# Kernel tuning notes

Measured on AMD Instinct MI355X. Metric: run time of the kernel, lower is better.

## Reference

```python
import jax, jax.numpy as jnp
import numpy as np

VOCAB = 32000
E = 512      # embed_dim
H = 512      # hidden_dim (== embed_dim, required by the output-averaging slice)
NUM_LAYERS = 2
WIN = 8
S = 512      # seq_len
B = 8        # batch


def setup_inputs() -> dict:
    key = jax.random.key(0)
    ks = jax.random.split(key, 40)
    d = {"encoder_input": jax.random.randint(ks[0], (S, B), 0, VOCAB, dtype=jnp.int64
                                             if jax.config.jax_enable_x64 else jnp.int32)}
    d["embed_table"] = jax.random.normal(ks[1], (VOCAB, E), jnp.float32) * 0.02
    i = 2
    for l in range(NUM_LAYERS):
        in_dim = E if l == 0 else 2 * H
        for dirn in ("f", "b"):
            sc = 1.0 / np.sqrt(H).astype(np.float32)
            d[f"wih{l}{dirn}"] = jax.random.normal(ks[i], (4 * H, in_dim), jnp.float32) * sc; i += 1
            d[f"whh{l}{dirn}"] = jax.random.normal(ks[i], (4 * H, H), jnp.float32) * sc; i += 1
            d[f"b{l}{dirn}"] = jax.random.normal(ks[i], (4 * H,), jnp.float32) * sc; i += 1
    return d


def _lstm_dir(x, mask, wih, whh, b, reverse):
    """One LSTM direction over padded windows. x: [L, N, in], mask: [L, N, 1].
    Masked (out-of-window) steps carry state unchanged; since invalid steps form a
    prefix in scan order (left pad for fwd, right pad for bwd-reversed), the zero
    initial state is preserved until the first valid step -> identical math to
    running the LSTM on the truncated window, as in the original per-token loop."""
    Hh = whh.shape[1]

    def step(carry, inp):
        h, c = carry
        xt, mt = inp
        g = xt @ wih.T + h @ whh.T + b                      # [N, 4H], torch gate order i,f,g,o
        i_, f_, g_, o_ = jnp.split(g, 4, axis=-1)
        c_new = jax.nn.sigmoid(f_) * c + jax.nn.sigmoid(i_) * jnp.tanh(g_)
        h_new = jax.nn.sigmoid(o_) * jnp.tanh(c_new)
        h = jnp.where(mt, h_new, h)
        c = jnp.where(mt, c_new, c)
        return (h, c), h

    N = x.shape[1]
    h0 = jnp.zeros((N, Hh), x.dtype)
    _, ys = jax.lax.scan(step, (h0, h0), (x, mask), reverse=reverse)
    return ys  # [L, N, Hh]


def _forward(encoder_input, embed_table, layer_params):
    S_, B_ = encoder_input.shape
    L = 2 * WIN + 1
    emb = embed_table[encoder_input]                         # [S, B, E]
    offs = jnp.arange(L) - WIN
    pos = jnp.arange(S_)[:, None] + offs[None, :]            # [S, L]
    valid = (pos >= 0) & (pos < S_)
    pidx = jnp.clip(pos, 0, S_ - 1)
    windows = emb[pidx]                                      # [S, L, B, E]
    x = windows.transpose(1, 0, 2, 3).reshape(L, S_ * B_, E)  # [L, N, E]
    mask = jnp.broadcast_to(valid.T[:, :, None, None], (L, S_, B_, 1)).reshape(L, S_ * B_, 1)
    for (wf, hf, bf, wb, hb, bb) in layer_params:
        yf = _lstm_dir(x, mask, wf, hf, bf, reverse=False)
        yb = _lstm_dir(x, mask, wb, hb, bb, reverse=True)
        x = jnp.concatenate([yf, yb], axis=-1)               # [L, N, 2H]
    out = x[WIN].reshape(S_, B_, 2 * H)                      # [S, B, 2H]
    return (out[:, :, :E] + out[:, :, E:]) / 2


def reference(encoder_input, embed_table,
              wih0f, whh0f, b0f, wih0b, whh0b, b0b,
              wih1f, whh1f, b1f, wih1b, whh1b, b1b):
    layer_params = [(wih0f, whh0f, b0f, wih0b, whh0b, b0b),
                    (wih1f, whh1f, b1f, wih1b, whh1b, b1b)]
    return _forward(encoder_input, embed_table, layer_params)
```

## Files before the change

kernel.cpp:

```cpp
#include <hip/hip_runtime.h>
#include <stdint.h>

typedef __bf16 bf16;
typedef __bf16 bf16x8 __attribute__((ext_vector_type(8)));
typedef __bf16 bf16x4 __attribute__((ext_vector_type(4)));
typedef float f32x4 __attribute__((ext_vector_type(4)));

#define WIN 8

__device__ __forceinline__ float sigm(float x) { return 1.0f / (1.0f + __expf(-x)); }
__device__ __forceinline__ float tanhfast(float x) { return 2.0f / (1.0f + __expf(-2.0f * x)) - 1.0f; }

__device__ __forceinline__ void gload16(const void* g, void* l) {
    __builtin_amdgcn_global_load_lds((const __attribute__((address_space(1))) void*)g,
                                     (__attribute__((address_space(3))) void*)l, 16, 0, 0);
}

struct StepArgs {
    const bf16* A1;
    const bf16* A2;
    const bf16* W;
    const float* bias;
    const bf16* P0;
    float* Cst;
    bf16* Hout;
    float* Hf32;
    const bf16* Hprev;
    int l;
    int firstStep;
};

template<int MODE>
__global__ __launch_bounds__(512, 2)
void step_pair(StepArgs fa, StepArgs ba) {
    const StepArgs a = blockIdx.z ? ba : fa;
    __shared__ alignas(16) char lds[131072];

    constexpr int SA1 = (MODE == 0) ? 512 : 1024;
    constexpr int SW  = (MODE == 2) ? 1536 : 512;
    constexpr int SH  = (MODE == 0) ? 2048 : (MODE == 1 ? 1024 : 512);
    constexpr int SHP = (MODE == 1) ? 1024 : 512;

    const int tid = threadIdx.x;
    const int w = tid >> 6;
    const int lane = tid & 63;
    const int wm = w >> 2, wn = w & 3;
    const int bx = blockIdx.x, by = blockIdx.y;
    const int rowBase = bx * 256;

    int KB;
    if (MODE == 0) KB = 8;
    else if (MODE == 1) KB = a.firstStep ? 0 : 8;
    else KB = a.firstStep ? 16 : 24;

    const int lq = lane >> 3;
    const int lc = lane & 7;
    const int swz = 8 * (lc ^ lq);

    const bf16* aP[4];
    const bf16* a2P[4];
    const bf16* bP[4];
#pragma unroll
    for (int q = 0; q < 4; ++q) {
        const int r = w * 32 + q * 8 + lq;
        const int n = rowBase + r;
        aP[q] = a.A1 ? (a.A1 + (size_t)n * SA1 + swz) : (const bf16*)0;
        if (MODE == 2) a2P[q] = a.A2 ? (a.A2 + (size_t)n * 512 + swz) : (const bf16*)0;
        int wr;
        if (MODE == 0) wr = by * 256 + r;
        else wr = ((r & 63) >> 4) * 512 + by * 64 + (r >> 6) * 16 + (r & 15);
        bP[q] = a.W + (size_t)wr * SW + swz;
    }

    const int l15 = lane & 15, l4 = lane >> 4;
    const int key = (l15 & 7) << 4;
    const int aBase = (wm * 128 + l15) * 128;
    const int bBase = (wn * 64 + l15) * 128;

    f32x4 acc[8][4];
    const f32x4 zf = {0.f, 0.f, 0.f, 0.f};
#pragma unroll
    for (int m = 0; m < 8; ++m)
#pragma unroll
        for (int n = 0; n < 4; ++n) acc[m][n] = zf;

    auto STAGE = [&](int buf, int kb) {
        char* Ad = lds + buf * 65536;
        char* Bd = Ad + 32768;
        const int ke = kb * 64;
        const int ldsOff0 = w * 32 * 128;
#pragma unroll
        for (int q = 0; q < 4; ++q) {
            const int ldsOff = ldsOff0 + q * 1024;
            const bf16* srcA;
            if (MODE == 2) srcA = (kb < 16) ? (aP[q] + ke) : (a2P[q] + (ke - 1024));
            else srcA = aP[q] + ke;
            gload16(srcA, Ad + ldsOff);
            gload16(bP[q] + ke, Bd + ldsOff);
        }
    };

    if (KB > 0) {
        STAGE(0, 0);
        for (int t = 0; t < KB; ++t) {
            const int cur = t & 1;
            if (t + 1 < KB) {
                STAGE(cur ^ 1, t + 1);
                asm volatile("s_waitcnt vmcnt(8)" ::: "memory");
            } else {
                asm volatile("s_waitcnt vmcnt(0)" ::: "memory");
            }
            __builtin_amdgcn_s_barrier();
            __builtin_amdgcn_sched_barrier(0);
            const char* Ab = lds + cur * 65536;
            const char* Bb = Ab + 32768;
            __builtin_amdgcn_s_setprio(1);
#pragma unroll
            for (int kk = 0; kk < 2; ++kk) {
                const int ko = (kk * 64 + l4 * 16) ^ key;
                bf16x8 af[8], bv[4];
#pragma unroll
                for (int m = 0; m < 8; ++m)
                    af[m] = *(const bf16x8*)(Ab + aBase + m * 2048 + ko);
#pragma unroll
                for (int n = 0; n < 4; ++n)
                    bv[n] = *(const bf16x8*)(Bb + bBase + n * 2048 + ko);
#pragma unroll
                for (int m = 0; m < 8; ++m)
#pragma unroll
                    for (int n = 0; n < 4; ++n)
                        acc[m][n] = __builtin_amdgcn_mfma_f32_16x16x32_bf16(af[m], bv[n], acc[m][n], 0, 0, 0);
            }
            __builtin_amdgcn_s_setprio(0);
            __builtin_amdgcn_sched_barrier(0);
            __builtin_amdgcn_s_barrier();
        }
    }

    if (MODE == 0) {
#pragma unroll
        for (int m = 0; m < 8; ++m)
#pragma unroll
            for (int n = 0; n < 4; ++n) {
                const int col = by * 256 + wn * 64 + n * 16 + l15;
#pragma unroll
                for (int e = 0; e < 4; ++e) {
                    const int row = rowBase + wm * 128 + m * 16 + l4 * 4 + e;
                    a.Hout[(size_t)row * SH + col] = (bf16)acc[m][n][e];
                }
            }
        return;
    }

    const int u = by * 64 + wn * 16 + l15;
    const float bi = a.bias[u];
    const float bff = a.bias[512 + u];
    const float bg = a.bias[1024 + u];
    const float bo = a.bias[1536 + u];
#pragma unroll
    for (int m = 0; m < 8; ++m) {
#pragma unroll
        for (int e = 0; e < 4; ++e) {
            const int n = rowBase + wm * 128 + m * 16 + l4 * 4 + e;
            const int s = n >> 3;
            const int p = s + a.l - WIN;
            const bool valid = ((unsigned)p < 512u);
            float gi = acc[m][0][e] + bi;
            float gf = acc[m][1][e] + bff;
            float gg = acc[m][2][e] + bg;
            float go = acc[m][3][e] + bo;
            if (MODE == 1) {
                const int pc = p < 0 ? 0 : (p > 511 ? 511 : p);
                const size_t pr = (size_t)(pc * 8 + (n & 7)) * 2048;
                gi += (float)a.P0[pr + u];
                gf += (float)a.P0[pr + 512 + u];
                gg += (float)a.P0[pr + 1024 + u];
                go += (float)a.P0[pr + 1536 + u];
            }
            const float cold = a.firstStep ? 0.0f : a.Cst[(size_t)n * 512 + u];
            const float cnew = sigm(gf) * cold + sigm(gi) * tanhfast(gg);
            const float hnew = sigm(go) * tanhfast(cnew);
            float hv, cv;
            if (valid) { hv = hnew; cv = cnew; }
            else {
                hv = a.Hprev ? (float)a.Hprev[(size_t)n * SHP + u] : 0.0f;
                cv = cold;
            }
            a.Cst[(size_t)n * 512 + u] = cv;
            a.Hout[(size_t)n * SH + u] = (bf16)hv;
            if (a.Hf32) a.Hf32[(size_t)n * 512 + u] = hv;
        }
    }
}

__global__ void embed_kernel(const int* __restrict__ tok, const float* __restrict__ tbl,
                             bf16* __restrict__ X0) {
    const int n = blockIdx.x;
    const int t = tok[n];
    const float4 v = ((const float4*)(tbl + (size_t)t * 512))[threadIdx.x];
    bf16x4 o = {(bf16)v.x, (bf16)v.y, (bf16)v.z, (bf16)v.w};
    ((bf16x4*)(X0 + (size_t)n * 512))[threadIdx.x] = o;
}

__global__ void cvt_kernel(const float* __restrict__ src, bf16* __restrict__ dst, int n4) {
    const int i = blockIdx.x * 256 + threadIdx.x;
    if (i < n4) {
        const float4 v = ((const float4*)src)[i];
        bf16x4 o = {(bf16)v.x, (bf16)v.y, (bf16)v.z, (bf16)v.w};
        ((bf16x4*)dst)[i] = o;
    }
}

__global__ void build_w1_kernel(const float* __restrict__ wih, const float* __restrict__ whh,
                                bf16* __restrict__ dst) {
    const int r = blockIdx.x;
    for (int k = threadIdx.x; k < 1536; k += 256) {
        const float v = (k < 1024) ? wih[(size_t)r * 1024 + k] : whh[(size_t)r * 512 + (k - 1024)];
        dst[(size_t)r * 1536 + k] = (bf16)v;
    }
}

__global__ void combine_kernel(const float* __restrict__ hf, const float* __restrict__ hb,
                               float* __restrict__ out) {
    const int i = blockIdx.x * 256 + threadIdx.x;
    const float4 x = ((const float4*)hf)[i];
    const float4 y = ((const float4*)hb)[i];
    float4 r;
    r.x = (x.x + y.x) * 0.5f;
    r.y = (x.y + y.y) * 0.5f;
    r.z = (x.z + y.z) * 0.5f;
    r.w = (x.w + y.w) * 0.5f;
    ((float4*)out)[i] = r;
}

extern "C" void kernel_launch(void* const* d_in, const int* in_sizes, int n_in,
                              void* d_out, int out_size, void* d_ws, size_t ws_size,
                              hipStream_t stream) {
    (void)in_sizes; (void)n_in; (void)out_size;
    const int*   tok   = (const int*)d_in[0];
    const float* tbl   = (const float*)d_in[1];
    const float* wih0f = (const float*)d_in[2];
    const float* whh0f = (const float*)d_in[3];
    const float* b0f   = (const float*)d_in[4];
    const float* wih0b = (const float*)d_in[5];
    const float* whh0b = (const float*)d_in[6];
    const float* b0b   = (const float*)d_in[7];
    const float* wih1f = (const float*)d_in[8];
    const float* whh1f = (const float*)d_in[9];
    const float* b1f   = (const float*)d_in[10];
    const float* wih1b = (const float*)d_in[11];
    const float* whh1b = (const float*)d_in[12];
    const float* b1b   = (const float*)d_in[13];

    char* ws = (char*)d_ws;
    size_t off = 0;
    auto alloc = [&](size_t bytes) -> char* {
        char* p = ws + off;
        off += (bytes + 255) & ~(size_t)255;
        return p;
    };
    bf16* wih0f_b = (bf16*)alloc((size_t)2048 * 512 * 2);
    bf16* wih0b_b = (bf16*)alloc((size_t)2048 * 512 * 2);
    bf16* whh0f_b = (bf16*)alloc((size_t)2048 * 512 * 2);
    bf16* whh0b_b = (bf16*)alloc((size_t)2048 * 512 * 2);
    bf16* w1f_b   = (bf16*)alloc((size_t)2048 * 1536 * 2);
    bf16* w1b_b   = (bf16*)alloc((size_t)2048 * 1536 * 2);
    bf16* X0      = (bf16*)alloc((size_t)4096 * 512 * 2);
    bf16* P0f     = (bf16*)alloc((size_t)4096 * 2048 * 2);
    bf16* P0b     = (bf16*)alloc((size_t)4096 * 2048 * 2);
    bf16* X1      = (bf16*)alloc((size_t)17 * 4096 * 1024 * 2);
    float* c0f    = (float*)alloc((size_t)4096 * 512 * 4);
    float* c0b    = (float*)alloc((size_t)4096 * 512 * 4);
    bf16* h1f0    = (bf16*)alloc((size_t)4096 * 512 * 2);
    bf16* h1f1    = (bf16*)alloc((size_t)4096 * 512 * 2);
    bf16* h1b0    = (bf16*)alloc((size_t)4096 * 512 * 2);
    bf16* h1b1    = (bf16*)alloc((size_t)4096 * 512 * 2);
    float* hf32f  = (float*)alloc((size_t)4096 * 512 * 4);
    float* hf32b  = (float*)alloc((size_t)4096 * 512 * 4);
    if (off > ws_size) return;

    bf16* h1f[2] = {h1f0, h1f1};
    bf16* h1b[2] = {h1b0, h1b1};

    cvt_kernel<<<1024, 256, 0, stream>>>(wih0f, wih0f_b, 262144);
    cvt_kernel<<<1024, 256, 0, stream>>>(wih0b, wih0b_b, 262144);
    cvt_kernel<<<1024, 256, 0, stream>>>(whh0f, whh0f_b, 262144);
    cvt_kernel<<<1024, 256, 0, stream>>>(whh0b, whh0b_b, 262144);
    build_w1_kernel<<<2048, 256, 0, stream>>>(wih1f, whh1f, w1f_b);
    build_w1_kernel<<<2048, 256, 0, stream>>>(wih1b, whh1b, w1b_b);
    embed_kernel<<<4096, 128, 0, stream>>>(tok, tbl, X0);

    dim3 g(16, 8, 2), blk(512, 1, 1);

    {
        StepArgs f{}, b{};
        f.A1 = X0; f.W = wih0f_b; f.Hout = P0f;
        b = f; b.W = wih0b_b; b.Hout = P0b;
        step_pair<0><<<g, blk, 0, stream>>>(f, b);
    }

    const size_t SLOT = (size_t)4096 * 1024;

    for (int i = 0; i <= 16; ++i) {
        const int lf = i, lb = 16 - i;
        StepArgs f{}, b{};
        f.A1 = (lf == 0) ? (const bf16*)0 : X1 + (size_t)(lf - 1) * SLOT;
        f.W = whh0f_b; f.bias = b0f; f.P0 = P0f; f.Cst = c0f;
        f.Hout = X1 + (size_t)lf * SLOT; f.Hprev = f.A1;
        f.l = lf; f.firstStep = (lf == 0) ? 1 : 0;
        b.A1 = (lb == 16) ? (const bf16*)0 : X1 + (size_t)(lb + 1) * SLOT + 512;
        b.W = whh0b_b; b.bias = b0b; b.P0 = P0b; b.Cst = c0b;
        b.Hout = X1 + (size_t)lb * SLOT + 512; b.Hprev = b.A1;
        b.l = lb; b.firstStep = (lb == 16) ? 1 : 0;
        step_pair<1><<<g, blk, 0, stream>>>(f, b);
    }

    for (int i = 0; i <= 8; ++i) {
        const int lf = i, lb = 16 - i;
        StepArgs f{}, b{};
        f.A1 = X1 + (size_t)lf * SLOT;
        f.A2 = (i == 0) ? (const bf16*)0 : h1f[(i + 1) & 1];
        f.W = w1f_b; f.bias = b1f; f.Cst = c0f;
        f.Hout = h1f[i & 1]; f.Hf32 = (i == 8) ? hf32f : (float*)0;
        f.Hprev = f.A2;
        f.l = lf; f.firstStep = (i == 0) ? 1 : 0;
        b.A1 = X1 + (size_t)lb * SLOT;
        b.A2 = (i == 0) ? (const bf16*)0 : h1b[(i + 1) & 1];
        b.W = w1b_b; b.bias = b1b; b.Cst = c0b;
        b.Hout = h1b[i & 1]; b.Hf32 = (i == 8) ? hf32b : (float*)0;
        b.Hprev = b.A2;
        b.l = lb; b.firstStep = (i == 0) ? 1 : 0;
        step_pair<2><<<g, blk, 0, stream>>>(f, b);
    }

    combine_kernel<<<2048, 256, 0, stream>>>(hf32f, hf32b, (float*)d_out);
}
```

Baseline: 1.146 ms.

## Shrink step GEMM tile to 128 rows, 256 threads, single-buffered LDS

Changes the per-step LSTM GEMM from a 256x256 tile with 8 waves and double-buffered LDS to a 128x256 tile with 4 waves, a single LDS buffer and plain __syncthreads. The grid doubles along rows so more blocks can run per CU (launch bounds 3) and the machine is filled better. In exchange it loses the overlap of global-to-LDS loads with MFMA work, drops the priority and scheduling hints, and each block reloads the weight tile for half as many rows.

```diff
diff --git a/kernel.cpp b/kernel.cpp
--- a/kernel.cpp
+++ b/kernel.cpp
@@ -31,10 +31,10 @@
 };
 
 template<int MODE>
-__global__ __launch_bounds__(512, 2)
+__global__ __launch_bounds__(256, 3)
 void step_pair(StepArgs fa, StepArgs ba) {
     const StepArgs a = blockIdx.z ? ba : fa;
-    __shared__ alignas(16) char lds[131072];
+    __shared__ alignas(16) char lds[49152];
 
     constexpr int SA1 = (MODE == 0) ? 512 : 1024;
     constexpr int SW  = (MODE == 2) ? 1536 : 512;
@@ -44,9 +44,8 @@
     const int tid = threadIdx.x;
     const int w = tid >> 6;
     const int lane = tid & 63;
-    const int wm = w >> 2, wn = w & 3;
     const int bx = blockIdx.x, by = blockIdx.y;
-    const int rowBase = bx * 256;
+    const int rowBase = bx * 128;
 
     int KB;
     if (MODE == 0) KB = 8;
@@ -59,13 +58,17 @@
 
     const bf16* aP[4];
     const bf16* a2P[4];
-    const bf16* bP[4];
 #pragma unroll
     for (int q = 0; q < 4; ++q) {
         const int r = w * 32 + q * 8 + lq;
         const int n = rowBase + r;
         aP[q] = a.A1 ? (a.A1 + (size_t)n * SA1 + swz) : (const bf16*)0;
         if (MODE == 2) a2P[q] = a.A2 ? (a.A2 + (size_t)n * 512 + swz) : (const bf16*)0;
+    }
+    const bf16* bP[8];
+#pragma unroll
+    for (int q = 0; q < 8; ++q) {
+        const int r = w * 64 + q * 8 + lq;
         int wr;
         if (MODE == 0) wr = by * 256 + r;
         else wr = ((r & 63) >> 4) * 512 + by * 64 + (r >> 6) * 16 + (r & 15);
@@ -74,8 +77,8 @@
 
     const int l15 = lane & 15, l4 = lane >> 4;
     const int key = (l15 & 7) << 4;
-    const int aBase = (wm * 128 + l15) * 128;
-    const int bBase = (wn * 64 + l15) * 128;
+    const int aBase = l15 * 128;
+    const int bBase = (w * 64 + l15) * 128;
 
     f32x4 acc[8][4];
     const f32x4 zf = {0.f, 0.f, 0.f, 0.f};
@@ -84,57 +87,43 @@
 #pragma unroll
         for (int n = 0; n < 4; ++n) acc[m][n] = zf;
 
-    auto STAGE = [&](int buf, int kb) {
-        char* Ad = lds + buf * 65536;
-        char* Bd = Ad + 32768;
+    char* Ad = lds;
+    char* Bd = lds + 16384;
+
+    auto STAGE = [&](int kb) {
         const int ke = kb * 64;
-        const int ldsOff0 = w * 32 * 128;
 #pragma unroll
         for (int q = 0; q < 4; ++q) {
-            const int ldsOff = ldsOff0 + q * 1024;
             const bf16* srcA;
             if (MODE == 2) srcA = (kb < 16) ? (aP[q] + ke) : (a2P[q] + (ke - 1024));
             else srcA = aP[q] + ke;
-            gload16(srcA, Ad + ldsOff);
-            gload16(bP[q] + ke, Bd + ldsOff);
+            gload16(srcA, Ad + (w * 32 + q * 8) * 128);
         }
+#pragma unroll
+        for (int q = 0; q < 8; ++q)
+            gload16(bP[q] + ke, Bd + (w * 64 + q * 8) * 128);
     };
 
-    if (KB > 0) {
-        STAGE(0, 0);
-        for (int t = 0; t < KB; ++t) {
-            const int cur = t & 1;
-            if (t + 1 < KB) {
-                STAGE(cur ^ 1, t + 1);
-                asm volatile("s_waitcnt vmcnt(8)" ::: "memory");
-            } else {
-                asm volatile("s_waitcnt vmcnt(0)" ::: "memory");
-            }
-            __builtin_amdgcn_s_barrier();
-            __builtin_amdgcn_sched_barrier(0);
-            const char* Ab = lds + cur * 65536;
-            const char* Bb = Ab + 32768;
-            __builtin_amdgcn_s_setprio(1);
-#pragma unroll
-            for (int kk = 0; kk < 2; ++kk) {
-                const int ko = (kk * 64 + l4 * 16) ^ key;
-                bf16x8 af[8], bv[4];
-#pragma unroll
-                for (int m = 0; m < 8; ++m)
-                    af[m] = *(const bf16x8*)(Ab + aBase + m * 2048 + ko);
+    for (int t = 0; t < KB; ++t) {
+        STAGE(t);
+        __syncthreads();
+#pragma unroll
+        for (int kk = 0; kk < 2; ++kk) {
+            const int ko = (kk * 64 + l4 * 16) ^ key;
+            bf16x8 af[8], bv[4];
+#pragma unroll
+            for (int m = 0; m < 8; ++m)
+                af[m] = *(const bf16x8*)(Ad + aBase + m * 2048 + ko);
+#pragma unroll
+            for (int n = 0; n < 4; ++n)
+                bv[n] = *(const bf16x8*)(Bd + bBase + n * 2048 + ko);
+#pragma unroll
+            for (int m = 0; m < 8; ++m)
 #pragma unroll
                 for (int n = 0; n < 4; ++n)
-                    bv[n] = *(const bf16x8*)(Bb + bBase + n * 2048 + ko);
-#pragma unroll
-                for (int m = 0; m < 8; ++m)
-#pragma unroll
-                    for (int n = 0; n < 4; ++n)
-                        acc[m][n] = __builtin_amdgcn_mfma_f32_16x16x32_bf16(af[m], bv[n], acc[m][n], 0, 0, 0);
-            }
-            __builtin_amdgcn_s_setprio(0);
-            __builtin_amdgcn_sched_barrier(0);
-            __builtin_amdgcn_s_barrier();
+                    acc[m][n] = __builtin_amdgcn_mfma_f32_16x16x32_bf16(af[m], bv[n], acc[m][n], 0, 0, 0);
         }
+        __syncthreads();
     }
 
     if (MODE == 0) {
@@ -142,17 +131,17 @@
         for (int m = 0; m < 8; ++m)
 #pragma unroll
             for (int n = 0; n < 4; ++n) {
-                const int col = by * 256 + wn * 64 + n * 16 + l15;
+                const int col = by * 256 + w * 64 + n * 16 + l15;
 #pragma unroll
                 for (int e = 0; e < 4; ++e) {
-                    const int row = rowBase + wm * 128 + m * 16 + l4 * 4 + e;
+                    const int row = rowBase + m * 16 + l4 * 4 + e;
                     a.Hout[(size_t)row * SH + col] = (bf16)acc[m][n][e];
                 }
             }
         return;
     }
 
-    const int u = by * 64 + wn * 16 + l15;
+    const int u = by * 64 + w * 16 + l15;
     const float bi = a.bias[u];
     const float bff = a.bias[512 + u];
     const float bg = a.bias[1024 + u];
@@ -161,7 +150,7 @@
     for (int m = 0; m < 8; ++m) {
 #pragma unroll
         for (int e = 0; e < 4; ++e) {
-            const int n = rowBase + wm * 128 + m * 16 + l4 * 4 + e;
+            const int n = rowBase + m * 16 + l4 * 4 + e;
             const int s = n >> 3;
             const int p = s + a.l - WIN;
             const bool valid = ((unsigned)p < 512u);
@@ -290,7 +279,7 @@
     build_w1_kernel<<<2048, 256, 0, stream>>>(wih1b, whh1b, w1b_b);
     embed_kernel<<<4096, 128, 0, stream>>>(tok, tbl, X0);
 
-    dim3 g(16, 8, 2), blk(512, 1, 1);
+    dim3 g(32, 8, 2), blk(256, 1, 1);
 
     {
         StepArgs f{}, b{};
```

Result: slower. 2.267 ms (+97.8%).

## Shrink step GEMM tile to 256x128 with 4 waves and split-phase prefetch

Applied to the files above, without the earlier changes.

Changes the per-step LSTM GEMM block from 512 threads with a 256x256 tile to 256 threads with a 256x128 tile. K-tiles shrink from 64 to 32 and LDS drops from 128KB to 48KB, with no XOR swizzle. Each K-iteration now runs two MFMA halves, and the prefetch of the next stage is interleaved between them. The grid doubles in y so more blocks fill the CUs, and the six weight-conversion launches are merged into one prep kernel. The risks are bank conflicts from the unswizzled LDS layout, more barriers per K, and lower operand reuse per block.

```diff
diff --git a/kernel.cpp b/kernel.cpp
--- a/kernel.cpp
+++ b/kernel.cpp
@@ -31,10 +31,10 @@
 };
 
 template<int MODE>
-__global__ __launch_bounds__(512, 2)
+__global__ __launch_bounds__(256, 2)
 void step_pair(StepArgs fa, StepArgs ba) {
     const StepArgs a = blockIdx.z ? ba : fa;
-    __shared__ alignas(16) char lds[131072];
+    __shared__ alignas(16) char lds[49152];
 
     constexpr int SA1 = (MODE == 0) ? 512 : 1024;
     constexpr int SW  = (MODE == 2) ? 1536 : 512;
@@ -44,38 +44,40 @@
     const int tid = threadIdx.x;
     const int w = tid >> 6;
     const int lane = tid & 63;
-    const int wm = w >> 2, wn = w & 3;
+    const int wm = w >> 1, wn = w & 1;
     const int bx = blockIdx.x, by = blockIdx.y;
     const int rowBase = bx * 256;
 
     int KB;
-    if (MODE == 0) KB = 8;
-    else if (MODE == 1) KB = a.firstStep ? 0 : 8;
-    else KB = a.firstStep ? 16 : 24;
-
-    const int lq = lane >> 3;
-    const int lc = lane & 7;
-    const int swz = 8 * (lc ^ lq);
+    if (MODE == 0) KB = 16;
+    else if (MODE == 1) KB = a.firstStep ? 0 : 16;
+    else KB = a.firstStep ? 32 : 48;
+
+    const int lr = lane >> 2;
+    const int lcB = (lane & 3) * 8;
 
     const bf16* aP[4];
     const bf16* a2P[4];
-    const bf16* bP[4];
-#pragma unroll
-    for (int q = 0; q < 4; ++q) {
-        const int r = w * 32 + q * 8 + lq;
+#pragma unroll
+    for (int j = 0; j < 4; ++j) {
+        const int r = w * 64 + j * 16 + lr;
         const int n = rowBase + r;
-        aP[q] = a.A1 ? (a.A1 + (size_t)n * SA1 + swz) : (const bf16*)0;
-        if (MODE == 2) a2P[q] = a.A2 ? (a.A2 + (size_t)n * 512 + swz) : (const bf16*)0;
+        aP[j] = a.A1 ? (a.A1 + (size_t)n * SA1 + lcB) : (const bf16*)0;
+        if (MODE == 2) a2P[j] = a.A2 ? (a.A2 + (size_t)n * 512 + lcB) : (const bf16*)0;
+    }
+    const bf16* bP[2];
+#pragma unroll
+    for (int j = 0; j < 2; ++j) {
+        const int r = w * 32 + j * 16 + lr;
         int wr;
-        if (MODE == 0) wr = by * 256 + r;
-        else wr = ((r & 63) >> 4) * 512 + by * 64 + (r >> 6) * 16 + (r & 15);
-        bP[q] = a.W + (size_t)wr * SW + swz;
+        if (MODE == 0) wr = by * 128 + r;
+        else wr = ((r >> 4) & 3) * 512 + by * 32 + (r >> 6) * 16 + (r & 15);
+        bP[j] = a.W + (size_t)wr * SW + lcB;
     }
 
     const int l15 = lane & 15, l4 = lane >> 4;
-    const int key = (l15 & 7) << 4;
-    const int aBase = (wm * 128 + l15) * 128;
-    const int bBase = (wn * 64 + l15) * 128;
+    const int aOffB = (wm * 128 + l15) * 64 + l4 * 16;
+    const int bOffB = (wn * 64 + l15) * 64 + l4 * 16;
 
     f32x4 acc[8][4];
     const f32x4 zf = {0.f, 0.f, 0.f, 0.f};
@@ -84,56 +86,70 @@
 #pragma unroll
         for (int n = 0; n < 4; ++n) acc[m][n] = zf;
 
-    auto STAGE = [&](int buf, int kb) {
-        char* Ad = lds + buf * 65536;
-        char* Bd = Ad + 32768;
-        const int ke = kb * 64;
-        const int ldsOff0 = w * 32 * 128;
-#pragma unroll
-        for (int q = 0; q < 4; ++q) {
-            const int ldsOff = ldsOff0 + q * 1024;
-            const bf16* srcA;
-            if (MODE == 2) srcA = (kb < 16) ? (aP[q] + ke) : (a2P[q] + (ke - 1024));
-            else srcA = aP[q] + ke;
-            gload16(srcA, Ad + ldsOff);
-            gload16(bP[q] + ke, Bd + ldsOff);
-        }
+    auto STAGE_A = [&](char* Sd, int kt, int j) {
+        const int ke = kt * 32;
+        const bf16* src;
+        if (MODE == 2) src = (kt < 32) ? (aP[j] + ke) : (a2P[j] + (ke - 1024));
+        else src = aP[j] + ke;
+        gload16(src, Sd + (w * 64 + j * 16) * 64);
     };
+    auto STAGE_B = [&](char* Sd, int kt, int j) {
+        gload16(bP[j] + kt * 32, Sd + 16384 + (w * 32 + j * 16) * 64);
+    };
 
     if (KB > 0) {
-        STAGE(0, 0);
+#pragma unroll
+        for (int j = 0; j < 4; ++j) STAGE_A(lds, 0, j);
+#pragma unroll
+        for (int j = 0; j < 2; ++j) STAGE_B(lds, 0, j);
+        asm volatile("s_waitcnt vmcnt(0)" ::: "memory");
+        __builtin_amdgcn_s_barrier();
+
         for (int t = 0; t < KB; ++t) {
             const int cur = t & 1;
-            if (t + 1 < KB) {
-                STAGE(cur ^ 1, t + 1);
-                asm volatile("s_waitcnt vmcnt(8)" ::: "memory");
-            } else {
-                asm volatile("s_waitcnt vmcnt(0)" ::: "memory");
-            }
+            const char* Ab = lds + cur * 24576;
+            const char* Bb = Ab + 16384;
+            char* Sd = lds + (cur ^ 1) * 24576;
+            const bool pf = (t + 1 < KB);
+            bf16x8 af[4], bv[4];
+
+            if (pf) { STAGE_A(Sd, t + 1, 0); STAGE_A(Sd, t + 1, 1); STAGE_B(Sd, t + 1, 0); }
+#pragma unroll
+            for (int i = 0; i < 4; ++i)
+                af[i] = *(const bf16x8*)(Ab + aOffB + i * 1024);
+#pragma unroll
+            for (int n = 0; n < 4; ++n)
+                bv[n] = *(const bf16x8*)(Bb + bOffB + n * 1024);
             __builtin_amdgcn_s_barrier();
+            asm volatile("s_waitcnt lgkmcnt(0)" ::: "memory");
             __builtin_amdgcn_sched_barrier(0);
-            const char* Ab = lds + cur * 65536;
-            const char* Bb = Ab + 32768;
             __builtin_amdgcn_s_setprio(1);
 #pragma unroll
-            for (int kk = 0; kk < 2; ++kk) {
-                const int ko = (kk * 64 + l4 * 16) ^ key;
-                bf16x8 af[8], bv[4];
-#pragma unroll
-                for (int m = 0; m < 8; ++m)
-                    af[m] = *(const bf16x8*)(Ab + aBase + m * 2048 + ko);
+            for (int i = 0; i < 4; ++i)
 #pragma unroll
                 for (int n = 0; n < 4; ++n)
-                    bv[n] = *(const bf16x8*)(Bb + bBase + n * 2048 + ko);
-#pragma unroll
-                for (int m = 0; m < 8; ++m)
-#pragma unroll
-                    for (int n = 0; n < 4; ++n)
-                        acc[m][n] = __builtin_amdgcn_mfma_f32_16x16x32_bf16(af[m], bv[n], acc[m][n], 0, 0, 0);
-            }
+                    acc[i][n] = __builtin_amdgcn_mfma_f32_16x16x32_bf16(af[i], bv[n], acc[i][n], 0, 0, 0);
             __builtin_amdgcn_s_setprio(0);
             __builtin_amdgcn_sched_barrier(0);
             __builtin_amdgcn_s_barrier();
+
+            if (pf) { STAGE_A(Sd, t + 1, 2); STAGE_A(Sd, t + 1, 3); STAGE_B(Sd, t + 1, 1); }
+#pragma unroll
+            for (int i = 0; i < 4; ++i)
+                af[i] = *(const bf16x8*)(Ab + aOffB + (4 + i) * 1024);
+            __builtin_amdgcn_s_barrier();
+            asm volatile("s_waitcnt lgkmcnt(0)" ::: "memory");
+            __builtin_amdgcn_sched_barrier(0);
+            __builtin_amdgcn_s_setprio(1);
+#pragma unroll
+            for (int i = 0; i < 4; ++i)
+#pragma unroll
+                for (int n = 0; n < 4; ++n)
+                    acc[4 + i][n] = __builtin_amdgcn_mfma_f32_16x16x32_bf16(af[i], bv[n], acc[4 + i][n], 0, 0, 0);
+            __builtin_amdgcn_s_setprio(0);
+            __builtin_amdgcn_sched_barrier(0);
+            if (pf) asm volatile("s_waitcnt vmcnt(0)" ::: "memory");
+            __builtin_amdgcn_s_barrier();
         }
     }
 
@@ -142,7 +158,7 @@
         for (int m = 0; m < 8; ++m)
 #pragma unroll
             for (int n = 0; n < 4; ++n) {
-                const int col = by * 256 + wn * 64 + n * 16 + l15;
+                const int col = by * 128 + wn * 64 + n * 16 + l15;
 #pragma unroll
                 for (int e = 0; e < 4; ++e) {
                     const int row = rowBase + wm * 128 + m * 16 + l4 * 4 + e;
@@ -152,7 +168,7 @@
         return;
     }
 
-    const int u = by * 64 + wn * 16 + l15;
+    const int u = by * 32 + wn * 16 + l15;
     const float bi = a.bias[u];
     const float bff = a.bias[512 + u];
     const float bg = a.bias[1024 + u];
@@ -202,21 +218,30 @@
     ((bf16x4*)(X0 + (size_t)n * 512))[threadIdx.x] = o;
 }
 
-__global__ void cvt_kernel(const float* __restrict__ src, bf16* __restrict__ dst, int n4) {
-    const int i = blockIdx.x * 256 + threadIdx.x;
-    if (i < n4) {
-        const float4 v = ((const float4*)src)[i];
-        bf16x4 o = {(bf16)v.x, (bf16)v.y, (bf16)v.z, (bf16)v.w};
-        ((bf16x4*)dst)[i] = o;
-    }
-}
-
-__global__ void build_w1_kernel(const float* __restrict__ wih, const float* __restrict__ whh,
-                                bf16* __restrict__ dst) {
+__global__ void prep_kernel(const float* __restrict__ wih0f, const float* __restrict__ wih0b,
+                            const float* __restrict__ whh0f, const float* __restrict__ whh0b,
+                            const float* __restrict__ wih1f, const float* __restrict__ whh1f,
+                            const float* __restrict__ wih1b, const float* __restrict__ whh1b,
+                            bf16* __restrict__ d0, bf16* __restrict__ d1,
+                            bf16* __restrict__ d2, bf16* __restrict__ d3,
+                            bf16* __restrict__ d4, bf16* __restrict__ d5) {
     const int r = blockIdx.x;
-    for (int k = threadIdx.x; k < 1536; k += 256) {
-        const float v = (k < 1024) ? wih[(size_t)r * 1024 + k] : whh[(size_t)r * 512 + (k - 1024)];
-        dst[(size_t)r * 1536 + k] = (bf16)v;
+    const int y = blockIdx.y;
+    if (y < 4) {
+        const float* s = (y == 0) ? wih0f : (y == 1) ? wih0b : (y == 2) ? whh0f : whh0b;
+        bf16* d = (y == 0) ? d0 : (y == 1) ? d1 : (y == 2) ? d2 : d3;
+        const int k = threadIdx.x * 2;
+        const float2 v = *(const float2*)(s + (size_t)r * 512 + k);
+        d[(size_t)r * 512 + k] = (bf16)v.x;
+        d[(size_t)r * 512 + k + 1] = (bf16)v.y;
+    } else {
+        const float* wih = (y == 4) ? wih1f : wih1b;
+        const float* whh = (y == 4) ? whh1f : whh1b;
+        bf16* d = (y == 4) ? d4 : d5;
+        for (int k = threadIdx.x; k < 1536; k += 256) {
+            const float v = (k < 1024) ? wih[(size_t)r * 1024 + k] : whh[(size_t)r * 512 + (k - 1024)];
+            d[(size_t)r * 1536 + k] = (bf16)v;
+        }
     }
 }
 
@@ -282,15 +307,13 @@
     bf16* h1f[2] = {h1f0, h1f1};
     bf16* h1b[2] = {h1b0, h1b1};
 
-    cvt_kernel<<<1024, 256, 0, stream>>>(wih0f, wih0f_b, 262144);
-    cvt_kernel<<<1024, 256, 0, stream>>>(wih0b, wih0b_b, 262144);
-    cvt_kernel<<<1024, 256, 0, stream>>>(whh0f, whh0f_b, 262144);
-    cvt_kernel<<<1024, 256, 0, stream>>>(whh0b, whh0b_b, 262144);
-    build_w1_kernel<<<2048, 256, 0, stream>>>(wih1f, whh1f, w1f_b);
-    build_w1_kernel<<<2048, 256, 0, stream>>>(wih1b, whh1b, w1b_b);
+    prep_kernel<<<dim3(2048, 6), 256, 0, stream>>>(wih0f, wih0b, whh0f, whh0b,
+                                                   wih1f, whh1f, wih1b, whh1b,
+                                                   wih0f_b, wih0b_b, whh0f_b, whh0b_b,
+                                                   w1f_b, w1b_b);
     embed_kernel<<<4096, 128, 0, stream>>>(tok, tbl, X0);
 
-    dim3 g(16, 8, 2), blk(512, 1, 1);
+    dim3 g(16, 16, 2), blk(256, 1, 1);
 
     {
         StepArgs f{}, b{};
```

New measurement: 1.236 ms. 7.8% more time.
